# Optimization experiments

Hardware: AMD Instinct MI355X
Metric: run time of the kernel (lower is better)

## Reference

```python
import jax, jax.numpy as jnp
import numpy as np

N = 50000
IN_DIM = 128
HIDDEN = 64
OUT_DIM = 10
HEADS = 4
NUM_LAYERS = 3
NEG_SLOPE = 0.2


def _glorot(key, shape):
    fan_in, fan_out = shape[0], shape[-1]
    lim = jnp.sqrt(6.0 / (fan_in + fan_out))
    return jax.random.uniform(key, shape, jnp.float32, -lim, lim)


def setup_inputs() -> dict:
    key = jax.random.key(0)
    ks = jax.random.split(key, 2 + 4 * NUM_LAYERS + 2)
    inp = {}
    inp["x"] = jax.random.normal(ks[0], (N, IN_DIM), jnp.float32)
    inp["edge_index"] = jax.random.randint(ks[1], (2, 800000), 0, N, jnp.int64)
    ki = 2
    for i in range(NUM_LAYERS):
        d_in = IN_DIM if i == 0 else HIDDEN
        inp[f"W{i}"] = _glorot(ks[ki], (d_in, HEADS * HIDDEN)); ki += 1
        inp[f"asrc{i}"] = _glorot(ks[ki], (HEADS, HIDDEN)); ki += 1
        inp[f"adst{i}"] = _glorot(ks[ki], (HEADS, HIDDEN)); ki += 1
        inp[f"b{i}"] = jnp.zeros((HIDDEN,), jnp.float32); ki += 1
    inp["fcW"] = _glorot(ks[ki], (HIDDEN, OUT_DIM)); ki += 1
    inp["fcb"] = jnp.zeros((OUT_DIM,), jnp.float32)
    return inp


def _gat_layer(x, W, a_src, a_dst, bias, src, dst):
    # x: [N, d_in] -> h: [N, H, D]
    h = (x @ W).reshape(N, HEADS, HIDDEN)
    al_s = jnp.einsum("nhd,hd->nh", h, a_src)  # [N, H]
    al_d = jnp.einsum("nhd,hd->nh", h, a_dst)  # [N, H]
    e = jax.nn.leaky_relu(al_s[src] + al_d[dst], NEG_SLOPE)  # [E, H]
    # segment softmax over incoming edges of each destination node
    m = jax.ops.segment_max(e, dst, num_segments=N)  # [N, H]
    ex = jnp.exp(e - m[dst])
    denom = jax.ops.segment_sum(ex, dst, num_segments=N)  # [N, H]
    alpha = ex / denom[dst]  # [E, H]
    # weighted scatter-add aggregation: [E,H,D] -> [N,H,D]
    out = jax.ops.segment_sum(alpha[:, :, None] * h[src], dst, num_segments=N)
    return out.mean(axis=1) + bias  # concat=False -> head mean, [N, HIDDEN]


def reference(x, edge_index, W0, asrc0, adst0, b0, W1, asrc1, adst1, b1,
              W2, asrc2, adst2, b2, fcW, fcb):
    # PyG GATConv default: add self-loops
    loops = jnp.arange(N, dtype=edge_index.dtype)
    src = jnp.concatenate([edge_index[0], loops])
    dst = jnp.concatenate([edge_index[1], loops])
    params = [(W0, asrc0, adst0, b0), (W1, asrc1, adst1, b1), (W2, asrc2, adst2, b2)]
    h = x
    for (W, a_s, a_d, b) in params:
        h = _gat_layer(h, W, a_s, a_d, b, src, dst)
        h = jax.nn.elu(h)
        # dropout p=0.3 is a no-op in eval mode
    return h @ fcW + fcb  # [N, OUT_DIM]
```

## Files before the change

### kernel.cpp

```cpp
#include <hip/hip_runtime.h>
#include <hip/hip_fp16.h>
#include <math.h>

#define N_NODES 50000
#define IN_DIM  128
#define HIDDEN  64
#define OUT_DIM 10
#define HEADS   4
#define E_RAW   800000
#define E_TOT   (E_RAW + N_NODES)
#define NEG_SLOPE 0.2f

#define NB_SCAN 196
#define NB_GEMH 782
#define NB_NODE 12500
#define NB_FILL 831

#define PAD 64

typedef _Float16 half8 __attribute__((ext_vector_type(8)));
typedef float floatx4 __attribute__((ext_vector_type(4)));

__global__ void prep_kernel(const int* __restrict__ ei, int* __restrict__ cnt,
                            int* __restrict__ flag,
                            const float* __restrict__ X, __half* __restrict__ Xh,
                            const float* __restrict__ W0, const float* __restrict__ W1,
                            const float* __restrict__ W2,
                            __half* __restrict__ Wtf0, __half* __restrict__ Wtf1,
                            __half* __restrict__ Wtf2,
                            const float* __restrict__ as0, const float* __restrict__ ad0,
                            const float* __restrict__ as1, const float* __restrict__ ad1,
                            const float* __restrict__ as2, const float* __restrict__ ad2,
                            float* __restrict__ Wa0, float* __restrict__ Wa1,
                            float* __restrict__ Wa2) {
    int bid = blockIdx.x, t = threadIdx.x;
    if (bid < 196) {
        int i = bid * 256 + t;
        if (i < N_NODES) {
            cnt[i] = 0;
            const float4* X4 = (const float4*)(X + (size_t)i * 128);
            __half2* xh2 = (__half2*)(Xh + (size_t)i * 128);
#pragma unroll 8
            for (int k4 = 0; k4 < 32; k4++) {
                float4 v = X4[k4];
                xh2[k4 * 2]     = __float22half2_rn(make_float2(v.x, v.y));
                xh2[k4 * 2 + 1] = __float22half2_rn(make_float2(v.z, v.w));
            }
        }
    } else if (bid == 196) {
        __shared__ int anyv;
        if (t == 0) anyv = 0;
        __syncthreads();
        int idx = 2 * (t * 3100 + 17) + 1;
        if (ei[idx] != 0) atomicOr(&anyv, 1);
        __syncthreads();
        if (t == 0) flag[0] = anyv;
    } else if (bid < 229) {
        int i = (bid - 197) * 256 + t;
        int KC, DIN, f;
        const float* W; __half* Wtf;
        if (i < 4096)      { f = i;        KC = 16; DIN = 128; W = W0; Wtf = Wtf0; }
        else if (i < 6144) { f = i - 4096; KC = 8;  DIN = 64;  W = W1; Wtf = Wtf1; }
        else if (i < 8192) { f = i - 6144; KC = 8;  DIN = 64;  W = W2; Wtf = Wtf2; }
        else return;
        int lane = f & 63, kc = (f >> 6) % KC, ct = f / (64 * KC);
        int m = lane & 15, quad = lane >> 4;
        int col = ct * 16 + m;
        __half tmp[8];
#pragma unroll
        for (int j = 0; j < 8; j++) {
            int k = kc * 32 + quad * 8 + j;
            int h = k / DIN, kk = k % DIN;
            tmp[j] = __float2half(0.25f * W[kk * 256 + h * 64 + col]);
        }
        *(uint4*)(Wtf + (size_t)f * 8) = *(uint4*)tmp;
    } else {
        int b = bid - 229;
        int l, k;
        if (b < 128)      { l = 0; k = b; }
        else if (b < 192) { l = 1; k = b - 128; }
        else              { l = 2; k = b - 192; }
        const float* W  = (l == 0) ? W0 : (l == 1) ? W1 : W2;
        const float* as = (l == 0) ? as0 : (l == 1) ? as1 : as2;
        const float* ad = (l == 0) ? ad0 : (l == 1) ? ad1 : ad2;
        float* Wa       = (l == 0) ? Wa0 : (l == 1) ? Wa1 : Wa2;
        int h = t >> 6, d = t & 63;
        float wv = W[k * 256 + h * 64 + d];
        float ss = wv * as[h * 64 + d];
        float dd = wv * ad[h * 64 + d];
#pragma unroll
        for (int o = 1; o < 64; o <<= 1) {
            ss += __shfl_xor(ss, o, 64);
            dd += __shfl_xor(dd, o, 64);
        }
        if (d == 0) {
            Wa[k * 8 + h]     = ss;
            Wa[k * 8 + 4 + h] = dd;
        }
    }
}


__device__ __forceinline__ void al128_body(
    int n, const float* __restrict__ X, const float* __restrict__ Wa,
    float* __restrict__ AL) {
    if (n >= N_NODES) return;
    const float4* X4 = (const float4*)(X + (size_t)n * 128);
    float s[8];
#pragma unroll
    for (int j = 0; j < 8; j++) s[j] = 0.f;
#pragma unroll 4
    for (int k4 = 0; k4 < 32; k4++) {
        float4 v = X4[k4];
#pragma unroll
        for (int j = 0; j < 8; j++)
            s[j] += v.x * Wa[(k4 * 4 + 0) * 8 + j] + v.y * Wa[(k4 * 4 + 1) * 8 + j]
                  + v.z * Wa[(k4 * 4 + 2) * 8 + j] + v.w * Wa[(k4 * 4 + 3) * 8 + j];
    }
    *(float4*)(AL + n * 8)     = make_float4(s[0], s[1], s[2], s[3]);
    *(float4*)(AL + n * 8 + 4) = make_float4(s[4], s[5], s[6], s[7]);
}

__global__ void __launch_bounds__(256) fill_al(
    const int* __restrict__ ei, int* __restrict__ cnt,
    int* __restrict__ esrc_pad, const int* __restrict__ flag,
    const float* __restrict__ X, const float* __restrict__ Wa0,
    float* __restrict__ AL) {
    if (blockIdx.x < NB_FILL) {
        int base = blockIdx.x * 1024 + threadIdx.x;
        int sh = flag[0] ? 0 : 1;
        int srcs[4], dsts[4], poss[4];
        bool valid[4];
#pragma unroll
        for (int j = 0; j < 4; j++) {
            int t = base + j * 256;
            valid[j] = (t < E_TOT);
            srcs[j] = 0; dsts[j] = 0;
            if (valid[j]) {
                if (t < E_RAW) { srcs[j] = ei[t << sh]; dsts[j] = ei[(E_RAW + t) << sh]; }
                else           { srcs[j] = t - E_RAW;   dsts[j] = srcs[j]; }
            }
        }
#pragma unroll
        for (int j = 0; j < 4; j++)
            if (valid[j]) poss[j] = atomicAdd(&cnt[dsts[j]], 1);
#pragma unroll
        for (int j = 0; j < 4; j++)
            if (valid[j] && poss[j] < PAD)
                esrc_pad[(dsts[j] << 6) + poss[j]] = srcs[j];
    } else {
        int n = (blockIdx.x - NB_FILL) * 256 + threadIdx.x;
        al128_body(n, X, Wa0, AL);
    }
}

__device__ __forceinline__ void agg_prologue(
    int n, int c, int wave, int lane,
    const float* __restrict__ AL, const int* __restrict__ esrc,
    float (*ldsE)[64][4], int (*ldsS)[64], float* dn) {
    const float4* AL4 = (const float4*)AL;
    float4 ad = AL4[n * 2 + 1];
    int my_s = 0;
    float4 myE = make_float4(0.f, 0.f, 0.f, 0.f);
    if (lane < c) {
        my_s = esrc[(n << 6) + lane];
        float4 as = AL4[my_s * 2];
        float v0 = as.x + ad.x; v0 = fmaxf(v0, NEG_SLOPE * v0);
        float v1 = as.y + ad.y; v1 = fmaxf(v1, NEG_SLOPE * v1);
        float v2 = as.z + ad.z; v2 = fmaxf(v2, NEG_SLOPE * v2);
        float v3 = as.w + ad.w; v3 = fmaxf(v3, NEG_SLOPE * v3);
        myE = make_float4(__expf(v0), __expf(v1), __expf(v2), __expf(v3));
    }
    *(float4*)&ldsE[wave][lane][0] = myE;
    ldsS[wave][lane] = my_s;
    float d0 = myE.x, d1 = myE.y, d2 = myE.z, d3 = myE.w;
#pragma unroll
    for (int o = 1; o < 64; o <<= 1) {
        d0 += __shfl_xor(d0, o, 64);
        d1 += __shfl_xor(d1, o, 64);
        d2 += __shfl_xor(d2, o, 64);
        d3 += __shfl_xor(d3, o, 64);
    }
    dn[0] = d0; dn[1] = d1; dn[2] = d2; dn[3] = d3;
}

__global__ void __launch_bounds__(256) agg_x128(
    const __half* __restrict__ X16, const float* __restrict__ AL,
    const int* __restrict__ cnt, const int* __restrict__ esrc,
    __half* __restrict__ AGG) {
    __shared__ float ldsE[4][64][4];
    __shared__ int   ldsS[4][64];
    int wave = threadIdx.x >> 6, lane = threadIdx.x & 63;
    int n = blockIdx.x * 4 + wave;
    int c = cnt[n]; if (c > PAD) c = PAD;

    float dn[4];
    agg_prologue(n, c, wave, lane, AL, esrc, ldsE, ldsS, dn);

    float acc0[4] = {0.f, 0.f, 0.f, 0.f};
    float acc1[4] = {0.f, 0.f, 0.f, 0.f};
    int lx = lane << 1;
    int nIter = (c + 7) >> 3;
    for (int it = 0; it < nIter; ++it) {
        int j0 = it << 3;
#pragma unroll
        for (int k = 0; k < 8; k++) {
            int sv = ldsS[wave][j0 + k];
            float2 xv = __half22float2(*(const __half2*)(X16 + (sv << 7) + lx));
            float4 E = *(const float4*)&ldsE[wave][j0 + k][0];
            acc0[0] += E.x * xv.x; acc0[1] += E.y * xv.x;
            acc0[2] += E.z * xv.x; acc0[3] += E.w * xv.x;
            acc1[0] += E.x * xv.y; acc1[1] += E.y * xv.y;
            acc1[2] += E.z * xv.y; acc1[3] += E.w * xv.y;
        }
    }
#pragma unroll
    for (int h = 0; h < 4; h++) {
        float inv = 1.f / dn[h];
        *(__half2*)(AGG + n * 512 + h * 128 + lx) =
            __float22half2_rn(make_float2(acc0[h] * inv, acc1[h] * inv));
    }
}

__global__ void __launch_bounds__(256) agg_x64(
    const __half* __restrict__ X16, const float* __restrict__ AL,
    const int* __restrict__ cnt, const int* __restrict__ esrc,
    __half* __restrict__ AGG) {
    __shared__ float ldsE[4][64][4];
    __shared__ int   ldsS[4][64];
    int wave = threadIdx.x >> 6, lane = threadIdx.x & 63;
    int n = blockIdx.x * 4 + wave;
    int c = cnt[n]; if (c > PAD) c = PAD;

    float dn[4];
    agg_prologue(n, c, wave, lane, AL, esrc, ldsE, ldsS, dn);

    int hlf = lane >> 5;
    int dp = lane & 31;
    int dx = dp << 1;
    float a0[4] = {0.f, 0.f, 0.f, 0.f};
    float a1[4] = {0.f, 0.f, 0.f, 0.f};
    int nIter = (c + 15) >> 4;
    for (int it = 0; it < nIter; ++it) {
        int e0 = (it << 4) + hlf;
#pragma unroll
        for (int k = 0; k < 8; k++) {
            int e = e0 + (k << 1);
            int sv = ldsS[wave][e];
            float2 xv = __half22float2(*(const __half2*)(X16 + (sv << 6) + dx));
            float4 E = *(const float4*)&ldsE[wave][e][0];
            a0[0] += E.x * xv.x; a0[1] += E.y * xv.x;
            a0[2] += E.z * xv.x; a0[3] += E.w * xv.x;
            a1[0] += E.x * xv.y; a1[1] += E.y * xv.y;
            a1[2] += E.z * xv.y; a1[3] += E.w * xv.y;
        }
    }
#pragma unroll
    for (int h = 0; h < 4; h++) {
        a0[h] += __shfl_xor(a0[h], 32, 64);
        a1[h] += __shfl_xor(a1[h], 32, 64);
    }
    int h0 = hlf << 1;
#pragma unroll
    for (int hh = 0; hh < 2; hh++) {
        int h = h0 + hh;
        float inv = 1.f / dn[h];
        *(__half2*)(AGG + n * 256 + h * 64 + dx) =
            __float22half2_rn(make_float2(a0[h] * inv, a1[h] * inv));
    }
}

template <int K>
__global__ void __launch_bounds__(256) gemm_out(
    const __half* __restrict__ AGG, const __half* __restrict__ Wtf,
    const float* __restrict__ bias, const float* __restrict__ Wa,
    float* __restrict__ XOUT, __half* __restrict__ X16,
    float* __restrict__ ALout) {
    __shared__ _Float16 lds[16384];
    const int KC = K / 32;
    const int NCHUNK = (K == 512) ? 2 : 1;
    const int CTC = 4 / NCHUNK;
    int t = threadIdx.x;
    int w = t >> 6, lane = t & 63;
    int m = lane & 15, quad = lane >> 4;
    int n0 = blockIdx.x * 64;
    int nr = n0 + w * 16 + m;
    int nc = (nr < N_NODES) ? nr : (N_NODES - 1);

    half8 afrag[KC];
#pragma unroll
    for (int kc = 0; kc < KC; kc++)
        afrag[kc] = *(const half8*)(AGG + (size_t)nc * K + kc * 32 + quad * 8);

    floatx4 accs[4];
    const uint4* Wg = (const uint4*)Wtf;
#pragma unroll
    for (int c = 0; c < NCHUNK; c++) {
        __syncthreads();
        uint4* dstl = (uint4*)lds;
        const uint4* srcg = Wg + (size_t)c * 2048;
#pragma unroll
        for (int q = 0; q < 8; q++) dstl[t + 256 * q] = srcg[t + 256 * q];
        __syncthreads();
#pragma unroll
        for (int ctl = 0; ctl < CTC; ctl++) {
            floatx4 acc = {0.f, 0.f, 0.f, 0.f};
#pragma unroll
            for (int kc = 0; kc < KC; kc++) {
                half8 b = *(const half8*)&lds[((ctl * KC + kc) * 64 + lane) * 8];
                acc = __builtin_amdgcn_mfma_f32_16x16x32_f16(afrag[kc], b, acc, 0, 0, 0);
            }
            accs[c * CTC + ctl] = acc;
        }
    }
    float vv[4][4];
#pragma unroll
    for (int ct = 0; ct < 4; ct++) {
        float bv = bias[ct * 16 + m];
#pragma unroll
        for (int i = 0; i < 4; i++) {
            float v = accs[ct][i] + bv;
            vv[ct][i] = v > 0.f ? v : (__expf(v) - 1.f);
        }
    }
    int nodeBase = n0 + w * 16 + quad * 4;
#pragma unroll
    for (int ct = 0; ct < 4; ct++) {
        int col = ct * 16 + m;
#pragma unroll
        for (int i = 0; i < 4; i++) {
            int node = nodeBase + i;
            if (node < N_NODES) {
                if (XOUT) XOUT[(size_t)node * 64 + col] = vv[ct][i];
                if (X16)  X16[(size_t)node * 64 + col] = __float2half(vv[ct][i]);
            }
        }
    }
    if (ALout) {
        float war[4][8];
#pragma unroll
        for (int ct = 0; ct < 4; ct++) {
            const float4* wp = (const float4*)(Wa + (ct * 16 + m) * 8);
            float4 a = wp[0], b = wp[1];
            war[ct][0] = a.x; war[ct][1] = a.y; war[ct][2] = a.z; war[ct][3] = a.w;
            war[ct][4] = b.x; war[ct][5] = b.y; war[ct][6] = b.z; war[ct][7] = b.w;
        }
#pragma unroll
        for (int i = 0; i < 4; i++) {
            int node = nodeBase + i;
            float alm = 0.f;
#pragma unroll
            for (int j = 0; j < 8; j++) {
                float s = vv[0][i] * war[0][j] + vv[1][i] * war[1][j]
                        + vv[2][i] * war[2][j] + vv[3][i] * war[3][j];
                s += __shfl_xor(s, 1, 64);
                s += __shfl_xor(s, 2, 64);
                s += __shfl_xor(s, 4, 64);
                s += __shfl_xor(s, 8, 64);
                if (j == (m & 7)) alm = s;
            }
            if (m < 8 && node < N_NODES) ALout[(size_t)node * 8 + m] = alm;
        }
    }
}

__global__ void __launch_bounds__(256) fc_kernel(
    const float* __restrict__ X, const float* __restrict__ fcW,
    const float* __restrict__ fcb, float* __restrict__ OUT) {
    __shared__ float ws[64 * 10];
    __shared__ float bs[10];
    int t = threadIdx.x;
    for (int i = t; i < 640; i += 256) ws[i] = fcW[i];
    if (t < 10) bs[t] = fcb[t];
    __syncthreads();
    int n = blockIdx.x * 256 + t;
    if (n >= N_NODES) return;
    float acc[10];
#pragma unroll
    for (int c = 0; c < 10; c++) acc[c] = bs[c];
    for (int d = 0; d < 64; d++) {
        float x = X[n * 64 + d];
#pragma unroll
        for (int c = 0; c < 10; c++) acc[c] += x * ws[d * 10 + c];
    }
#pragma unroll
    for (int c = 0; c < 10; c++) OUT[n * 10 + c] = acc[c];
}

extern "C" void kernel_launch(void* const* d_in, const int* in_sizes, int n_in,
                              void* d_out, int out_size, void* d_ws, size_t ws_size,
                              hipStream_t stream) {
    const float* x     = (const float*)d_in[0];
    const int*   ei    = (const int*)d_in[1];
    const float* W[3]    = {(const float*)d_in[2], (const float*)d_in[6], (const float*)d_in[10]};
    const float* asrc[3] = {(const float*)d_in[3], (const float*)d_in[7], (const float*)d_in[11]};
    const float* adst[3] = {(const float*)d_in[4], (const float*)d_in[8], (const float*)d_in[12]};
    const float* bias[3] = {(const float*)d_in[5], (const float*)d_in[9], (const float*)d_in[13]};
    const float* fcW = (const float*)d_in[14];
    const float* fcb = (const float*)d_in[15];
    float* out = (float*)d_out;

    char* ws = (char*)d_ws;
    size_t off = 0;
    auto alloc = [&](size_t bytes) {
        void* p = ws + off;
        off = (off + bytes + 255) & ~(size_t)255;
        return p;
    };
    __half* AGG     = (__half*)alloc((size_t)N_NODES * 512 * 2);
    float*  AL      = (float*)alloc((size_t)N_NODES * 8 * 4);
    float*  XA      = (float*)alloc((size_t)N_NODES * 64 * 4);
    __half* Xh0     = (__half*)alloc((size_t)N_NODES * 128 * 2);
    __half* X16     = (__half*)alloc((size_t)N_NODES * 64 * 2);
    __half* Wtf0    = (__half*)alloc(4096 * 8 * 2);
    __half* Wtf1    = (__half*)alloc(2048 * 8 * 2);
    __half* Wtf2    = (__half*)alloc(2048 * 8 * 2);
    float*  Wa0     = (float*)alloc(128 * 8 * 4);
    float*  Wa1     = (float*)alloc(64 * 8 * 4);
    float*  Wa2     = (float*)alloc(64 * 8 * 4);
    int* cnt      = (int*)alloc((size_t)N_NODES * 4);
    int* esrc_pad = (int*)alloc((size_t)N_NODES * PAD * 4);
    int* flag     = (int*)alloc(256 * 4);

    prep_kernel<<<485, 256, 0, stream>>>(ei, cnt, flag, x, Xh0,
                                         W[0], W[1], W[2],
                                         Wtf0, Wtf1, Wtf2,
                                         asrc[0], adst[0], asrc[1], adst[1],
                                         asrc[2], adst[2], Wa0, Wa1, Wa2);
    fill_al<<<NB_FILL + NB_SCAN, 256, 0, stream>>>(ei, cnt, esrc_pad, flag,
                                                   x, Wa0, AL);
    agg_x128<<<NB_NODE, 256, 0, stream>>>(Xh0, AL, cnt, esrc_pad, AGG);
    gemm_out<512><<<NB_GEMH, 256, 0, stream>>>(AGG, Wtf0, bias[0], Wa1,
                                               nullptr, X16, AL);
    agg_x64<<<NB_NODE, 256, 0, stream>>>(X16, AL, cnt, esrc_pad, AGG);
    gemm_out<256><<<NB_GEMH, 256, 0, stream>>>(AGG, Wtf1, bias[1], Wa2,
                                               nullptr, X16, AL);
    agg_x64<<<NB_NODE, 256, 0, stream>>>(X16, AL, cnt, esrc_pad, AGG);
    gemm_out<256><<<NB_GEMH, 256, 0, stream>>>(AGG, Wtf2, bias[2], nullptr,
                                               XA, nullptr, nullptr);

    fc_kernel<<<NB_SCAN, 256, 0, stream>>>(XA, fcW, fcb, out);
}
```

Before: 323.5 us.

## Fuse per-layer aggregation, projection GEMM, attention logits and final FC into one kernel

Merges the edge-aggregation kernel and the MFMA projection kernel for each GAT layer into a single 1024-thread block that handles 32 nodes. The aggregated rows stay in LDS instead of going through a global AGG buffer. The next layer's attention logits and the final FC are computed in the same kernel from an LDS tile, and X16/AL are double-buffered so the next layer's inputs are not overwritten while another block still reads them. The fill kernel also processes 8 edges per thread instead of 4. In exchange, each block has 16 waves but only 8 of them do MFMA work, there are extra block-wide barriers, and the large blocks may lower occupancy and latency hiding in the gather phase.

```diff
diff --git a/kernel.cpp b/kernel.cpp
--- a/kernel.cpp
+++ b/kernel.cpp
@@ -12,9 +12,8 @@
 #define NEG_SLOPE 0.2f
 
 #define NB_SCAN 196
-#define NB_GEMH 782
-#define NB_NODE 12500
-#define NB_FILL 831
+#define NB_FILL 416
+#define NB_AGG  1563
 
 #define PAD 64
 
@@ -127,12 +126,12 @@
     const float* __restrict__ X, const float* __restrict__ Wa0,
     float* __restrict__ AL) {
     if (blockIdx.x < NB_FILL) {
-        int base = blockIdx.x * 1024 + threadIdx.x;
+        int base = blockIdx.x * 2048 + threadIdx.x;
         int sh = flag[0] ? 0 : 1;
-        int srcs[4], dsts[4], poss[4];
-        bool valid[4];
-#pragma unroll
-        for (int j = 0; j < 4; j++) {
+        int srcs[8], dsts[8], poss[8];
+        bool valid[8];
+#pragma unroll
+        for (int j = 0; j < 8; j++) {
             int t = base + j * 256;
             valid[j] = (t < E_TOT);
             srcs[j] = 0; dsts[j] = 0;
@@ -142,10 +141,10 @@
             }
         }
 #pragma unroll
-        for (int j = 0; j < 4; j++)
+        for (int j = 0; j < 8; j++)
             if (valid[j]) poss[j] = atomicAdd(&cnt[dsts[j]], 1);
 #pragma unroll
-        for (int j = 0; j < 4; j++)
+        for (int j = 0; j < 8; j++)
             if (valid[j] && poss[j] < PAD)
                 esrc_pad[(dsts[j] << 6) + poss[j]] = srcs[j];
     } else {
@@ -155,7 +154,7 @@
 }
 
 __device__ __forceinline__ void agg_prologue(
-    int n, int c, int wave, int lane,
+    int n, int c, int w, int lane,
     const float* __restrict__ AL, const int* __restrict__ esrc,
     float (*ldsE)[64][4], int (*ldsS)[64], float* dn) {
     const float4* AL4 = (const float4*)AL;
@@ -171,8 +170,8 @@
         float v3 = as.w + ad.w; v3 = fmaxf(v3, NEG_SLOPE * v3);
         myE = make_float4(__expf(v0), __expf(v1), __expf(v2), __expf(v3));
     }
-    *(float4*)&ldsE[wave][lane][0] = myE;
-    ldsS[wave][lane] = my_s;
+    *(float4*)&ldsE[w][lane][0] = myE;
+    ldsS[w][lane] = my_s;
     float d0 = myE.x, d1 = myE.y, d2 = myE.z, d3 = myE.w;
 #pragma unroll
     for (int o = 1; o < 64; o <<= 1) {
@@ -184,207 +183,138 @@
     dn[0] = d0; dn[1] = d1; dn[2] = d2; dn[3] = d3;
 }
 
-__global__ void __launch_bounds__(256) agg_x128(
-    const __half* __restrict__ X16, const float* __restrict__ AL,
+template <int DIN>
+__global__ void __launch_bounds__(1024) agg_gemm(
+    const __half* __restrict__ Xin, const float* __restrict__ ALin,
     const int* __restrict__ cnt, const int* __restrict__ esrc,
-    __half* __restrict__ AGG) {
-    __shared__ float ldsE[4][64][4];
-    __shared__ int   ldsS[4][64];
-    int wave = threadIdx.x >> 6, lane = threadIdx.x & 63;
-    int n = blockIdx.x * 4 + wave;
-    int c = cnt[n]; if (c > PAD) c = PAD;
-
-    float dn[4];
-    agg_prologue(n, c, wave, lane, AL, esrc, ldsE, ldsS, dn);
-
-    float acc0[4] = {0.f, 0.f, 0.f, 0.f};
-    float acc1[4] = {0.f, 0.f, 0.f, 0.f};
-    int lx = lane << 1;
-    int nIter = (c + 7) >> 3;
-    for (int it = 0; it < nIter; ++it) {
-        int j0 = it << 3;
-#pragma unroll
-        for (int k = 0; k < 8; k++) {
-            int sv = ldsS[wave][j0 + k];
-            float2 xv = __half22float2(*(const __half2*)(X16 + (sv << 7) + lx));
-            float4 E = *(const float4*)&ldsE[wave][j0 + k][0];
-            acc0[0] += E.x * xv.x; acc0[1] += E.y * xv.x;
-            acc0[2] += E.z * xv.x; acc0[3] += E.w * xv.x;
-            acc1[0] += E.x * xv.y; acc1[1] += E.y * xv.y;
-            acc1[2] += E.z * xv.y; acc1[3] += E.w * xv.y;
-        }
-    }
-#pragma unroll
-    for (int h = 0; h < 4; h++) {
-        float inv = 1.f / dn[h];
-        *(__half2*)(AGG + n * 512 + h * 128 + lx) =
-            __float22half2_rn(make_float2(acc0[h] * inv, acc1[h] * inv));
-    }
-}
-
-__global__ void __launch_bounds__(256) agg_x64(
-    const __half* __restrict__ X16, const float* __restrict__ AL,
-    const int* __restrict__ cnt, const int* __restrict__ esrc,
-    __half* __restrict__ AGG) {
-    __shared__ float ldsE[4][64][4];
-    __shared__ int   ldsS[4][64];
-    int wave = threadIdx.x >> 6, lane = threadIdx.x & 63;
-    int n = blockIdx.x * 4 + wave;
-    int c = cnt[n]; if (c > PAD) c = PAD;
-
-    float dn[4];
-    agg_prologue(n, c, wave, lane, AL, esrc, ldsE, ldsS, dn);
-
-    int hlf = lane >> 5;
-    int dp = lane & 31;
-    int dx = dp << 1;
-    float a0[4] = {0.f, 0.f, 0.f, 0.f};
-    float a1[4] = {0.f, 0.f, 0.f, 0.f};
-    int nIter = (c + 15) >> 4;
-    for (int it = 0; it < nIter; ++it) {
-        int e0 = (it << 4) + hlf;
-#pragma unroll
-        for (int k = 0; k < 8; k++) {
-            int e = e0 + (k << 1);
-            int sv = ldsS[wave][e];
-            float2 xv = __half22float2(*(const __half2*)(X16 + (sv << 6) + dx));
-            float4 E = *(const float4*)&ldsE[wave][e][0];
-            a0[0] += E.x * xv.x; a0[1] += E.y * xv.x;
-            a0[2] += E.z * xv.x; a0[3] += E.w * xv.x;
-            a1[0] += E.x * xv.y; a1[1] += E.y * xv.y;
-            a1[2] += E.z * xv.y; a1[3] += E.w * xv.y;
-        }
-    }
-#pragma unroll
-    for (int h = 0; h < 4; h++) {
-        a0[h] += __shfl_xor(a0[h], 32, 64);
-        a1[h] += __shfl_xor(a1[h], 32, 64);
-    }
-    int h0 = hlf << 1;
-#pragma unroll
-    for (int hh = 0; hh < 2; hh++) {
-        int h = h0 + hh;
-        float inv = 1.f / dn[h];
-        *(__half2*)(AGG + n * 256 + h * 64 + dx) =
-            __float22half2_rn(make_float2(a0[h] * inv, a1[h] * inv));
-    }
-}
-
-template <int K>
-__global__ void __launch_bounds__(256) gemm_out(
-    const __half* __restrict__ AGG, const __half* __restrict__ Wtf,
-    const float* __restrict__ bias, const float* __restrict__ Wa,
-    float* __restrict__ XOUT, __half* __restrict__ X16,
-    float* __restrict__ ALout) {
-    __shared__ _Float16 lds[16384];
+    const __half* __restrict__ Wtf, const float* __restrict__ bias,
+    const float* __restrict__ WaN, __half* __restrict__ Xout,
+    float* __restrict__ ALout, const float* __restrict__ fcW,
+    const float* __restrict__ fcb, float* __restrict__ OUT) {
+    const int K  = DIN * 4;
+    const int RS = K + 8;
     const int KC = K / 32;
-    const int NCHUNK = (K == 512) ? 2 : 1;
-    const int CTC = 4 / NCHUNK;
-    int t = threadIdx.x;
-    int w = t >> 6, lane = t & 63;
-    int m = lane & 15, quad = lane >> 4;
-    int n0 = blockIdx.x * 64;
-    int nr = n0 + w * 16 + m;
-    int nc = (nr < N_NODES) ? nr : (N_NODES - 1);
-
-    half8 afrag[KC];
-#pragma unroll
-    for (int kc = 0; kc < KC; kc++)
-        afrag[kc] = *(const half8*)(AGG + (size_t)nc * K + kc * 32 + quad * 8);
-
-    floatx4 accs[4];
-    const uint4* Wg = (const uint4*)Wtf;
-#pragma unroll
-    for (int c = 0; c < NCHUNK; c++) {
-        __syncthreads();
-        uint4* dstl = (uint4*)lds;
-        const uint4* srcg = Wg + (size_t)c * 2048;
-#pragma unroll
-        for (int q = 0; q < 8; q++) dstl[t + 256 * q] = srcg[t + 256 * q];
-        __syncthreads();
-#pragma unroll
-        for (int ctl = 0; ctl < CTC; ctl++) {
-            floatx4 acc = {0.f, 0.f, 0.f, 0.f};
-#pragma unroll
-            for (int kc = 0; kc < KC; kc++) {
-                half8 b = *(const half8*)&lds[((ctl * KC + kc) * 64 + lane) * 8];
-                acc = __builtin_amdgcn_mfma_f32_16x16x32_f16(afrag[kc], b, acc, 0, 0, 0);
+    __shared__ __half aggT[32][DIN * 4 + 8];
+    __shared__ float  ldsE[16][64][4];
+    __shared__ int    ldsS[16][64];
+    __shared__ float  vvT[32][68];
+
+    int w = threadIdx.x >> 6, lane = threadIdx.x & 63;
+    int nbase = blockIdx.x * 32;
+
+    for (int nn = 0; nn < 2; nn++) {
+        int n = nbase + w * 2 + nn;
+        int ln = w * 2 + nn;
+        if (n < N_NODES) {
+            int c = cnt[n]; if (c > PAD) c = PAD;
+            float dn[4];
+            agg_prologue(n, c, w, lane, ALin, esrc, ldsE, ldsS, dn);
+            if (DIN == 128) {
+                float acc0[4] = {0.f,0.f,0.f,0.f}, acc1[4] = {0.f,0.f,0.f,0.f};
+                int lx = lane << 1;
+                int nIter = (c + 7) >> 3;
+                for (int it = 0; it < nIter; ++it) {
+                    int j0 = it << 3;
+#pragma unroll
+                    for (int k = 0; k < 8; k++) {
+                        int sv = ldsS[w][j0 + k];
+                        float2 xv = __half22float2(*(const __half2*)(Xin + (sv << 7) + lx));
+                        const float* E = ldsE[w][j0 + k];
+                        float e0 = E[0], e1 = E[1], e2 = E[2], e3 = E[3];
+                        acc0[0] += e0*xv.x; acc0[1] += e1*xv.x;
+                        acc0[2] += e2*xv.x; acc0[3] += e3*xv.x;
+                        acc1[0] += e0*xv.y; acc1[1] += e1*xv.y;
+                        acc1[2] += e2*xv.y; acc1[3] += e3*xv.y;
+                    }
+                }
+#pragma unroll
+                for (int h = 0; h < 4; h++) {
+                    float inv = 1.f / dn[h];
+                    *(__half2*)&aggT[ln][h * 128 + lx] =
+                        __float22half2_rn(make_float2(acc0[h]*inv, acc1[h]*inv));
+                }
+            } else {
+                int hlf = lane >> 5, dp = lane & 31, dx = dp << 1;
+                float a0[4] = {0.f,0.f,0.f,0.f}, a1[4] = {0.f,0.f,0.f,0.f};
+                int nIter = (c + 15) >> 4;
+                for (int it = 0; it < nIter; ++it) {
+                    int e0b = (it << 4) + hlf;
+#pragma unroll
+                    for (int k = 0; k < 8; k++) {
+                        int e = e0b + (k << 1);
+                        int sv = ldsS[w][e];
+                        float2 xv = __half22float2(*(const __half2*)(Xin + (sv << 6) + dx));
+                        const float* E = ldsE[w][e];
+                        float e0 = E[0], e1 = E[1], e2 = E[2], e3 = E[3];
+                        a0[0] += e0*xv.x; a0[1] += e1*xv.x;
+                        a0[2] += e2*xv.x; a0[3] += e3*xv.x;
+                        a1[0] += e0*xv.y; a1[1] += e1*xv.y;
+                        a1[2] += e2*xv.y; a1[3] += e3*xv.y;
+                    }
+                }
+#pragma unroll
+                for (int h = 0; h < 4; h++) {
+                    a0[h] += __shfl_xor(a0[h], 32, 64);
+                    a1[h] += __shfl_xor(a1[h], 32, 64);
+                }
+                int h0 = hlf << 1;
+#pragma unroll
+                for (int hh = 0; hh < 2; hh++) {
+                    int h = h0 + hh;
+                    float inv = 1.f / dn[h];
+                    *(__half2*)&aggT[ln][h * 64 + dx] =
+                        __float22half2_rn(make_float2(a0[h]*inv, a1[h]*inv));
+                }
             }
-            accs[c * CTC + ctl] = acc;
-        }
-    }
-    float vv[4][4];
-#pragma unroll
-    for (int ct = 0; ct < 4; ct++) {
-        float bv = bias[ct * 16 + m];
+        }
+    }
+    __syncthreads();
+
+    if (w < 8) {
+        int r = w & 1, ct = w >> 1;
+        int m = lane & 15, quad = lane >> 4;
+        floatx4 acc = {0.f, 0.f, 0.f, 0.f};
+#pragma unroll
+        for (int kc = 0; kc < KC; kc++) {
+            half8 a = *(const half8*)&aggT[r * 16 + m][kc * 32 + quad * 8];
+            half8 b = *(const half8*)(Wtf + (size_t)((ct * KC + kc) * 64 + lane) * 8);
+            acc = __builtin_amdgcn_mfma_f32_16x16x32_f16(a, b, acc, 0, 0, 0);
+        }
+        int col = ct * 16 + m;
+        float bv = bias[col];
 #pragma unroll
         for (int i = 0; i < 4; i++) {
-            float v = accs[ct][i] + bv;
-            vv[ct][i] = v > 0.f ? v : (__expf(v) - 1.f);
-        }
-    }
-    int nodeBase = n0 + w * 16 + quad * 4;
-#pragma unroll
-    for (int ct = 0; ct < 4; ct++) {
-        int col = ct * 16 + m;
-#pragma unroll
-        for (int i = 0; i < 4; i++) {
-            int node = nodeBase + i;
-            if (node < N_NODES) {
-                if (XOUT) XOUT[(size_t)node * 64 + col] = vv[ct][i];
-                if (X16)  X16[(size_t)node * 64 + col] = __float2half(vv[ct][i]);
-            }
-        }
-    }
-    if (ALout) {
-        float war[4][8];
-#pragma unroll
-        for (int ct = 0; ct < 4; ct++) {
-            const float4* wp = (const float4*)(Wa + (ct * 16 + m) * 8);
-            float4 a = wp[0], b = wp[1];
-            war[ct][0] = a.x; war[ct][1] = a.y; war[ct][2] = a.z; war[ct][3] = a.w;
-            war[ct][4] = b.x; war[ct][5] = b.y; war[ct][6] = b.z; war[ct][7] = b.w;
-        }
-#pragma unroll
-        for (int i = 0; i < 4; i++) {
-            int node = nodeBase + i;
-            float alm = 0.f;
-#pragma unroll
-            for (int j = 0; j < 8; j++) {
-                float s = vv[0][i] * war[0][j] + vv[1][i] * war[1][j]
-                        + vv[2][i] * war[2][j] + vv[3][i] * war[3][j];
-                s += __shfl_xor(s, 1, 64);
-                s += __shfl_xor(s, 2, 64);
-                s += __shfl_xor(s, 4, 64);
-                s += __shfl_xor(s, 8, 64);
-                if (j == (m & 7)) alm = s;
-            }
-            if (m < 8 && node < N_NODES) ALout[(size_t)node * 8 + m] = alm;
-        }
-    }
-}
-
-__global__ void __launch_bounds__(256) fc_kernel(
-    const float* __restrict__ X, const float* __restrict__ fcW,
-    const float* __restrict__ fcb, float* __restrict__ OUT) {
-    __shared__ float ws[64 * 10];
-    __shared__ float bs[10];
-    int t = threadIdx.x;
-    for (int i = t; i < 640; i += 256) ws[i] = fcW[i];
-    if (t < 10) bs[t] = fcb[t];
+            int lr = r * 16 + quad * 4 + i;
+            int node = nbase + lr;
+            float v = acc[i] + bv;
+            v = v > 0.f ? v : (__expf(v) - 1.f);
+            vvT[lr][col] = v;
+            if (Xout && node < N_NODES)
+                Xout[(size_t)node * 64 + col] = __float2half(v);
+        }
+    }
     __syncthreads();
-    int n = blockIdx.x * 256 + t;
-    if (n >= N_NODES) return;
-    float acc[10];
-#pragma unroll
-    for (int c = 0; c < 10; c++) acc[c] = bs[c];
-    for (int d = 0; d < 64; d++) {
-        float x = X[n * 64 + d];
-#pragma unroll
-        for (int c = 0; c < 10; c++) acc[c] += x * ws[d * 10 + c];
-    }
-#pragma unroll
-    for (int c = 0; c < 10; c++) OUT[n * 10 + c] = acc[c];
+
+    if (ALout != nullptr && threadIdx.x < 256) {
+        int nl = threadIdx.x >> 3, j = threadIdx.x & 7;
+        int node = nbase + nl;
+        if (node < N_NODES) {
+            float s = 0.f;
+#pragma unroll 8
+            for (int d = 0; d < 64; d++) s += vvT[nl][d] * WaN[d * 8 + j];
+            ALout[(size_t)node * 8 + j] = s;
+        }
+    }
+    if (OUT != nullptr && threadIdx.x < 320) {
+        int nl = threadIdx.x / 10, c = threadIdx.x % 10;
+        int node = nbase + nl;
+        if (node < N_NODES) {
+            float s = fcb[c];
+#pragma unroll 8
+            for (int d = 0; d < 64; d++) s += vvT[nl][d] * fcW[d * 10 + c];
+            OUT[(size_t)node * 10 + c] = s;
+        }
+    }
 }
 
 extern "C" void kernel_launch(void* const* d_in, const int* in_sizes, int n_in,
@@ -407,11 +337,11 @@
         off = (off + bytes + 255) & ~(size_t)255;
         return p;
     };
-    __half* AGG     = (__half*)alloc((size_t)N_NODES * 512 * 2);
-    float*  AL      = (float*)alloc((size_t)N_NODES * 8 * 4);
-    float*  XA      = (float*)alloc((size_t)N_NODES * 64 * 4);
+    float*  ALa     = (float*)alloc((size_t)N_NODES * 8 * 4);
+    float*  ALb     = (float*)alloc((size_t)N_NODES * 8 * 4);
     __half* Xh0     = (__half*)alloc((size_t)N_NODES * 128 * 2);
-    __half* X16     = (__half*)alloc((size_t)N_NODES * 64 * 2);
+    __half* X16a    = (__half*)alloc((size_t)N_NODES * 64 * 2);
+    __half* X16b    = (__half*)alloc((size_t)N_NODES * 64 * 2);
     __half* Wtf0    = (__half*)alloc(4096 * 8 * 2);
     __half* Wtf1    = (__half*)alloc(2048 * 8 * 2);
     __half* Wtf2    = (__half*)alloc(2048 * 8 * 2);
@@ -428,16 +358,14 @@
                                          asrc[0], adst[0], asrc[1], adst[1],
                                          asrc[2], adst[2], Wa0, Wa1, Wa2);
     fill_al<<<NB_FILL + NB_SCAN, 256, 0, stream>>>(ei, cnt, esrc_pad, flag,
-                                                   x, Wa0, AL);
-    agg_x128<<<NB_NODE, 256, 0, stream>>>(Xh0, AL, cnt, esrc_pad, AGG);
-    gemm_out<512><<<NB_GEMH, 256, 0, stream>>>(AGG, Wtf0, bias[0], Wa1,
-                                               nullptr, X16, AL);
-    agg_x64<<<NB_NODE, 256, 0, stream>>>(X16, AL, cnt, esrc_pad, AGG);
-    gemm_out<256><<<NB_GEMH, 256, 0, stream>>>(AGG, Wtf1, bias[1], Wa2,
-                                               nullptr, X16, AL);
-    agg_x64<<<NB_NODE, 256, 0, stream>>>(X16, AL, cnt, esrc_pad, AGG);
-    gemm_out<256><<<NB_GEMH, 256, 0, stream>>>(AGG, Wtf2, bias[2], nullptr,
-                                               XA, nullptr, nullptr);
-
-    fc_kernel<<<NB_SCAN, 256, 0, stream>>>(XA, fcW, fcb, out);
-}
+                                                   x, Wa0, ALa);
+    agg_gemm<128><<<NB_AGG, 1024, 0, stream>>>(
+        Xh0, ALa, cnt, esrc_pad, Wtf0, bias[0], Wa1,
+        X16a, ALb, nullptr, nullptr, nullptr);
+    agg_gemm<64><<<NB_AGG, 1024, 0, stream>>>(
+        X16a, ALb, cnt, esrc_pad, Wtf1, bias[1], Wa2,
+        X16b, ALa, nullptr, nullptr, nullptr);
+    agg_gemm<64><<<NB_AGG, 1024, 0, stream>>>(
+        X16b, ALa, cnt, esrc_pad, Wtf2, bias[2], nullptr,
+        nullptr, nullptr, fcW, fcb, out);
+}
```

Result: slower. 379.1 us (+17.2%).
